# Performance work log

Hardware: AMD Instinct MI355X
Metric: run time of the kernel (lower is better)

## Reference

```python
import jax, jax.numpy as jnp
import numpy as np

B, S, H, E, TOP_K = 4, 4096, 4096, 64, 2

def setup_inputs() -> dict:
    key = jax.random.key(0)
    k1, k2 = jax.random.split(key)
    hidden_states = jax.random.normal(k1, (B, S, H), dtype=jnp.float32)
    gate_weight = jax.random.normal(k2, (E, H), dtype=jnp.float32) * (H ** -0.5)
    return {"hidden_states": hidden_states, "gate_weight": gate_weight}

def reference(hidden_states, gate_weight):
    # gate: logits[b,s,e] = hidden[b,s,h] @ W[e,h]^T (nn.Linear, no bias)
    router_logits = jnp.einsum('bsh,eh->bse', hidden_states, gate_weight)
    router_probs = jax.nn.softmax(router_logits, axis=-1)
    # top-k over experts, then renormalize the selected weights
    expert_weights, expert_indices = jax.lax.top_k(router_probs, TOP_K)
    expert_weights = expert_weights / jnp.sum(expert_weights, axis=-1, keepdims=True)
    return (router_probs, expert_indices, expert_weights)
```

## Files before the change

kernel.cpp:

```cpp
#include <hip/hip_runtime.h>
#include <math.h>

#define TOKENS 16384
#define HDIM 4096
#define NE 64

#define BM 64
#define BK 64
#define LP 68

typedef float f32x4 __attribute__((ext_vector_type(4)));
typedef int i32x4 __attribute__((ext_vector_type(4)));
typedef __bf16 bf16x8 __attribute__((ext_vector_type(8)));

__device__ __forceinline__ void split8(f32x4 v0, f32x4 v1, i32x4& h, i32x4& l) {
  float x[8];
#pragma unroll
  for (int j = 0; j < 4; ++j) { x[j] = v0[j]; x[4 + j] = v1[j]; }
  union { unsigned short u[8]; i32x4 v; } H, L;
#pragma unroll
  for (int j = 0; j < 8; ++j) {
    __bf16 hb = (__bf16)x[j];
    H.u[j] = __builtin_bit_cast(unsigned short, hb);
    L.u[j] = __builtin_bit_cast(unsigned short, (__bf16)(x[j] - (float)hb));
  }
  h = H.v; l = L.v;
}

__device__ __forceinline__ f32x4 mfma_bf16(i32x4 a, i32x4 b, f32x4 c) {
  return __builtin_amdgcn_mfma_f32_16x16x32_bf16(
      __builtin_bit_cast(bf16x8, a), __builtin_bit_cast(bf16x8, b), c, 0, 0, 0);
}

__global__ __launch_bounds__(256) void convert_w(const float* __restrict__ W,
                                                 unsigned short* __restrict__ Wh,
                                                 unsigned short* __restrict__ Wl) {
  const int i = (blockIdx.x * 256 + threadIdx.x) * 8;
  f32x4 v0 = *(const f32x4*)(W + i);
  f32x4 v1 = *(const f32x4*)(W + i + 4);
  i32x4 h, l;
  split8(v0, v1, h, l);
  *(i32x4*)(Wh + i) = h;
  *(i32x4*)(Wl + i) = l;
}

__global__ __launch_bounds__(512, 2) void router_mfma(const float* __restrict__ A,
                                                      const unsigned short* __restrict__ Wh,
                                                      const unsigned short* __restrict__ Wl,
                                                      float* __restrict__ out) {
  __shared__ __align__(16) unsigned short smem[4 * BM * BK];
  unsigned short* AhS = smem;
  unsigned short* AlS = smem + BM * BK;
  unsigned short* WhS = smem + 2 * BM * BK;
  unsigned short* WlS = smem + 3 * BM * BK;

  const int tid = threadIdx.x;
  const int bt = blockIdx.x;

  const int srow = tid >> 3;
  const int sc = tid & 7;
  const int soff = srow * BK + ((sc ^ (srow & 7)) << 3);

  const float* Ab = A + (size_t)(bt * BM + srow) * HDIM + sc * 8;
  const unsigned short* Whb = Wh + srow * HDIM + sc * 8;
  const unsigned short* Wlb = Wl + srow * HDIM + sc * 8;

  const int lane = tid & 63;
  const int wv = tid >> 6;
  const int tg = wv & 3;
  const int eg = wv >> 2;
  const int l15 = lane & 15;
  const int l7 = lane & 7;
  const int fko = lane >> 4;
  const int arow = tg * 16 + l15;
  const int brow = eg * 32 + l15;

  f32x4 acc0 = {0.f, 0.f, 0.f, 0.f};
  f32x4 acc1 = {0.f, 0.f, 0.f, 0.f};

  f32x4 a0 = *(const f32x4*)(Ab);
  f32x4 a1 = *(const f32x4*)(Ab + 4);
  i32x4 whr = *(const i32x4*)(Whb);
  i32x4 wlr = *(const i32x4*)(Wlb);

  for (int kc = BK;; kc += BK) {
    i32x4 ah, al;
    split8(a0, a1, ah, al);
    *(i32x4*)&AhS[soff] = ah;
    *(i32x4*)&AlS[soff] = al;
    *(i32x4*)&WhS[soff] = whr;
    *(i32x4*)&WlS[soff] = wlr;
    __syncthreads();

    if (kc < HDIM) {
      a0 = *(const f32x4*)(Ab + kc);
      a1 = *(const f32x4*)(Ab + kc + 4);
      whr = *(const i32x4*)(Whb + kc);
      wlr = *(const i32x4*)(Wlb + kc);
    }

#pragma unroll
    for (int ks = 0; ks < 2; ++ks) {
      const int ch = ks * 4 + fko;
      const int aoff = arow * BK + ((ch ^ l7) << 3);
      const int boff = brow * BK + ((ch ^ l7) << 3);
      i32x4 fah = *(const i32x4*)&AhS[aoff];
      i32x4 fal = *(const i32x4*)&AlS[aoff];
      i32x4 fbh0 = *(const i32x4*)&WhS[boff];
      i32x4 fbl0 = *(const i32x4*)&WlS[boff];
      i32x4 fbh1 = *(const i32x4*)&WhS[boff + 16 * BK];
      i32x4 fbl1 = *(const i32x4*)&WlS[boff + 16 * BK];
      acc0 = mfma_bf16(fah, fbh0, acc0);
      acc1 = mfma_bf16(fah, fbh1, acc1);
      acc0 = mfma_bf16(fal, fbh0, acc0);
      acc1 = mfma_bf16(fal, fbh1, acc1);
      acc0 = mfma_bf16(fah, fbl0, acc0);
      acc1 = mfma_bf16(fah, fbl1, acc1);
      acc0 = mfma_bf16(fal, fbl0, acc0);
      acc1 = mfma_bf16(fal, fbl1, acc1);
    }
    if (kc >= HDIM) break;
    __syncthreads();
  }

  __syncthreads();
  float* L = (float*)smem;
#pragma unroll
  for (int r = 0; r < 4; ++r) {
    const int row = tg * 16 + fko * 4 + r;
    L[row * LP + eg * 32 + l15] = acc0[r];
    L[row * LP + eg * 32 + 16 + l15] = acc1[r];
  }
  __syncthreads();

  const int wv8 = tid >> 6;
#pragma unroll
  for (int r = 0; r < 8; ++r) {
    const int lt = wv8 * 8 + r;
    const int tok = bt * BM + lt;
    const float l = L[lt * LP + lane];

    float m = l;
#pragma unroll
    for (int off = 32; off >= 1; off >>= 1) m = fmaxf(m, __shfl_xor(m, off, 64));

    const float e = expf(l - m);
    float sum = e;
#pragma unroll
    for (int off = 32; off >= 1; off >>= 1) sum += __shfl_xor(sum, off, 64);

    const float p = e / sum;
    out[(size_t)tok * NE + lane] = p;

    float m0 = p;
#pragma unroll
    for (int off = 32; off >= 1; off >>= 1) m0 = fmaxf(m0, __shfl_xor(m0, off, 64));
    const unsigned long long b0 = __ballot(p == m0);
    const int i0 = __ffsll(b0) - 1;

    const float pm = (lane == i0) ? -1.f : p;
    float m1 = pm;
#pragma unroll
    for (int off = 32; off >= 1; off >>= 1) m1 = fmaxf(m1, __shfl_xor(m1, off, 64));
    const unsigned long long b1 = __ballot(pm == m1);
    const int i1 = __ffsll(b1) - 1;

    if (lane == 0) {
      float* idxo = out + (size_t)TOKENS * NE + (size_t)tok * 2;
      idxo[0] = (float)i0;
      idxo[1] = (float)i1;
      float* wo = out + (size_t)TOKENS * NE + (size_t)TOKENS * 2 + (size_t)tok * 2;
      const float d = m0 + m1;
      wo[0] = m0 / d;
      wo[1] = m1 / d;
    }
  }
}

extern "C" void kernel_launch(void* const* d_in, const int* in_sizes, int n_in,
                              void* d_out, int out_size, void* d_ws, size_t ws_size,
                              hipStream_t stream) {
  const float* A = (const float*)d_in[0];
  const float* W = (const float*)d_in[1];
  float* out = (float*)d_out;
  unsigned short* Whi = (unsigned short*)d_ws;
  unsigned short* Wlo = Whi + (size_t)NE * HDIM;

  convert_w<<<dim3(NE * HDIM / (256 * 8)), 256, 0, stream>>>(W, Whi, Wlo);
  router_mfma<<<dim3(TOKENS / BM), 512, 0, stream>>>(A, Whi, Wlo, out);
}
```

Before: 395.6 us.

## Double-buffer LDS tiles and drop lo*lo MFMA term in split-bf16 GEMM

Changes the router GEMM main loop to ping-pong between two LDS buffers. Staging the next tile overlaps with MFMA on the current one, which cuts the barrier count per K-step from two to one. It also removes the low×low bf16 product from the three-term split, so each step issues 6 MFMAs instead of 8. That slightly lowers accuracy, and the doubled LDS (64KB per block) may reduce occupancy.

```diff
diff --git a/kernel.cpp b/kernel.cpp
--- a/kernel.cpp
+++ b/kernel.cpp
@@ -7,7 +7,9 @@
 
 #define BM 64
 #define BK 64
+#define NT (HDIM / BK)
 #define LP 68
+#define TSZ (BM * BK)
 
 typedef float f32x4 __attribute__((ext_vector_type(4)));
 typedef int i32x4 __attribute__((ext_vector_type(4)));
@@ -48,11 +50,9 @@
                                                       const unsigned short* __restrict__ Wh,
                                                       const unsigned short* __restrict__ Wl,
                                                       float* __restrict__ out) {
-  __shared__ __align__(16) unsigned short smem[4 * BM * BK];
-  unsigned short* AhS = smem;
-  unsigned short* AlS = smem + BM * BK;
-  unsigned short* WhS = smem + 2 * BM * BK;
-  unsigned short* WlS = smem + 3 * BM * BK;
+  __shared__ __align__(16) unsigned short smem[2 * 4 * TSZ];
+  unsigned short* buf0 = smem;
+  unsigned short* buf1 = smem + 4 * TSZ;
 
   const int tid = threadIdx.x;
   const int bt = blockIdx.x;
@@ -78,27 +78,31 @@
   f32x4 acc0 = {0.f, 0.f, 0.f, 0.f};
   f32x4 acc1 = {0.f, 0.f, 0.f, 0.f};
 
-  f32x4 a0 = *(const f32x4*)(Ab);
-  f32x4 a1 = *(const f32x4*)(Ab + 4);
-  i32x4 whr = *(const i32x4*)(Whb);
-  i32x4 wlr = *(const i32x4*)(Wlb);
-
-  for (int kc = BK;; kc += BK) {
-    i32x4 ah, al;
-    split8(a0, a1, ah, al);
-    *(i32x4*)&AhS[soff] = ah;
-    *(i32x4*)&AlS[soff] = al;
-    *(i32x4*)&WhS[soff] = whr;
-    *(i32x4*)&WlS[soff] = wlr;
-    __syncthreads();
-
-    if (kc < HDIM) {
-      a0 = *(const f32x4*)(Ab + kc);
-      a1 = *(const f32x4*)(Ab + kc + 4);
-      whr = *(const i32x4*)(Whb + kc);
-      wlr = *(const i32x4*)(Wlb + kc);
-    }
-
+  f32x4 a0_0, a1_0, a0_1, a1_1;
+  i32x4 wh_0, wl_0, wh_1, wl_1;
+
+  auto loadS = [&](int t, f32x4& a0, f32x4& a1, i32x4& wh, i32x4& wl) {
+    const int kc = t * BK;
+    a0 = *(const f32x4*)(Ab + kc);
+    a1 = *(const f32x4*)(Ab + kc + 4);
+    wh = *(const i32x4*)(Whb + kc);
+    wl = *(const i32x4*)(Wlb + kc);
+  };
+
+  auto stage = [&](unsigned short* B, f32x4 a0, f32x4 a1, i32x4 wh, i32x4 wl) {
+    i32x4 h, l;
+    split8(a0, a1, h, l);
+    *(i32x4*)&B[soff] = h;
+    *(i32x4*)&B[TSZ + soff] = l;
+    *(i32x4*)&B[2 * TSZ + soff] = wh;
+    *(i32x4*)&B[3 * TSZ + soff] = wl;
+  };
+
+  auto compute = [&](const unsigned short* B) {
+    const unsigned short* AhS = B;
+    const unsigned short* AlS = B + TSZ;
+    const unsigned short* WhS = B + 2 * TSZ;
+    const unsigned short* WlS = B + 3 * TSZ;
 #pragma unroll
     for (int ks = 0; ks < 2; ++ks) {
       const int ch = ks * 4 + fko;
@@ -107,8 +111,8 @@
       i32x4 fah = *(const i32x4*)&AhS[aoff];
       i32x4 fal = *(const i32x4*)&AlS[aoff];
       i32x4 fbh0 = *(const i32x4*)&WhS[boff];
+      i32x4 fbh1 = *(const i32x4*)&WhS[boff + 16 * BK];
       i32x4 fbl0 = *(const i32x4*)&WlS[boff];
-      i32x4 fbh1 = *(const i32x4*)&WhS[boff + 16 * BK];
       i32x4 fbl1 = *(const i32x4*)&WlS[boff + 16 * BK];
       acc0 = mfma_bf16(fah, fbh0, acc0);
       acc1 = mfma_bf16(fah, fbh1, acc1);
@@ -116,14 +120,26 @@
       acc1 = mfma_bf16(fal, fbh1, acc1);
       acc0 = mfma_bf16(fah, fbl0, acc0);
       acc1 = mfma_bf16(fah, fbl1, acc1);
-      acc0 = mfma_bf16(fal, fbl0, acc0);
-      acc1 = mfma_bf16(fal, fbl1, acc1);
     }
-    if (kc >= HDIM) break;
+  };
+
+  loadS(0, a0_0, a1_0, wh_0, wl_0);
+  stage(buf0, a0_0, a1_0, wh_0, wl_0);
+  loadS(1, a0_1, a1_1, wh_1, wl_1);
+  __syncthreads();
+
+  for (int t = 0; t < NT; t += 2) {
+    compute(buf0);
+    if (t + 2 < NT) loadS(t + 2, a0_0, a1_0, wh_0, wl_0);
+    stage(buf1, a0_1, a1_1, wh_1, wl_1);
     __syncthreads();
-  }
-
-  __syncthreads();
+
+    compute(buf1);
+    if (t + 3 < NT) loadS(t + 3, a0_1, a1_1, wh_1, wl_1);
+    if (t + 2 < NT) stage(buf0, a0_0, a1_0, wh_0, wl_0);
+    __syncthreads();
+  }
+
   float* L = (float*)smem;
 #pragma unroll
   for (int r = 0; r < 4; ++r) {
```

New measurement: 394.2 us. About the same (-0.4%).

## Load MFMA fragments directly from global memory, drop LDS staging and low-low term

Applied to the files above, without the earlier changes.

Replaces the LDS-staged, double-synchronised K loop with per-wave direct global loads of A and W fragments into MFMA operand registers, removing shared-memory writes, reads and barriers. It also drops the lo*lo bf16 product, cutting MFMAs per step from 8 to 6. In exchange A is fetched and split by two waves, W is reread by four waves, global access is less coalesced, and the split-bf16 accuracy drops slightly.

```diff
diff --git a/kernel.cpp b/kernel.cpp
--- a/kernel.cpp
+++ b/kernel.cpp
@@ -6,7 +6,6 @@
 #define NE 64
 
 #define BM 64
-#define BK 64
 #define LP 68
 
 typedef float f32x4 __attribute__((ext_vector_type(4)));
@@ -48,83 +47,44 @@
                                                       const unsigned short* __restrict__ Wh,
                                                       const unsigned short* __restrict__ Wl,
                                                       float* __restrict__ out) {
-  __shared__ __align__(16) unsigned short smem[4 * BM * BK];
-  unsigned short* AhS = smem;
-  unsigned short* AlS = smem + BM * BK;
-  unsigned short* WhS = smem + 2 * BM * BK;
-  unsigned short* WlS = smem + 3 * BM * BK;
+  __shared__ __align__(16) float L[BM * LP];
 
   const int tid = threadIdx.x;
   const int bt = blockIdx.x;
-
-  const int srow = tid >> 3;
-  const int sc = tid & 7;
-  const int soff = srow * BK + ((sc ^ (srow & 7)) << 3);
-
-  const float* Ab = A + (size_t)(bt * BM + srow) * HDIM + sc * 8;
-  const unsigned short* Whb = Wh + srow * HDIM + sc * 8;
-  const unsigned short* Wlb = Wl + srow * HDIM + sc * 8;
-
   const int lane = tid & 63;
   const int wv = tid >> 6;
   const int tg = wv & 3;
   const int eg = wv >> 2;
   const int l15 = lane & 15;
-  const int l7 = lane & 7;
   const int fko = lane >> 4;
-  const int arow = tg * 16 + l15;
-  const int brow = eg * 32 + l15;
+
+  const float* Ap = A + (size_t)(bt * BM + tg * 16 + l15) * HDIM + fko * 8;
+  const unsigned short* Wh0 = Wh + (size_t)(eg * 32 + l15) * HDIM + fko * 8;
+  const unsigned short* Wl0 = Wl + (size_t)(eg * 32 + l15) * HDIM + fko * 8;
+  const unsigned short* Wh1 = Wh0 + 16 * HDIM;
+  const unsigned short* Wl1 = Wl0 + 16 * HDIM;
 
   f32x4 acc0 = {0.f, 0.f, 0.f, 0.f};
   f32x4 acc1 = {0.f, 0.f, 0.f, 0.f};
 
-  f32x4 a0 = *(const f32x4*)(Ab);
-  f32x4 a1 = *(const f32x4*)(Ab + 4);
-  i32x4 whr = *(const i32x4*)(Whb);
-  i32x4 wlr = *(const i32x4*)(Wlb);
-
-  for (int kc = BK;; kc += BK) {
+#pragma unroll 2
+  for (int kc = 0; kc < HDIM; kc += 32) {
+    f32x4 a0 = *(const f32x4*)(Ap + kc);
+    f32x4 a1 = *(const f32x4*)(Ap + kc + 4);
+    i32x4 wh0 = *(const i32x4*)(Wh0 + kc);
+    i32x4 wh1 = *(const i32x4*)(Wh1 + kc);
+    i32x4 wl0 = *(const i32x4*)(Wl0 + kc);
+    i32x4 wl1 = *(const i32x4*)(Wl1 + kc);
     i32x4 ah, al;
     split8(a0, a1, ah, al);
-    *(i32x4*)&AhS[soff] = ah;
-    *(i32x4*)&AlS[soff] = al;
-    *(i32x4*)&WhS[soff] = whr;
-    *(i32x4*)&WlS[soff] = wlr;
-    __syncthreads();
-
-    if (kc < HDIM) {
-      a0 = *(const f32x4*)(Ab + kc);
-      a1 = *(const f32x4*)(Ab + kc + 4);
-      whr = *(const i32x4*)(Whb + kc);
-      wlr = *(const i32x4*)(Wlb + kc);
-    }
-
-#pragma unroll
-    for (int ks = 0; ks < 2; ++ks) {
-      const int ch = ks * 4 + fko;
-      const int aoff = arow * BK + ((ch ^ l7) << 3);
-      const int boff = brow * BK + ((ch ^ l7) << 3);
-      i32x4 fah = *(const i32x4*)&AhS[aoff];
-      i32x4 fal = *(const i32x4*)&AlS[aoff];
-      i32x4 fbh0 = *(const i32x4*)&WhS[boff];
-      i32x4 fbl0 = *(const i32x4*)&WlS[boff];
-      i32x4 fbh1 = *(const i32x4*)&WhS[boff + 16 * BK];
-      i32x4 fbl1 = *(const i32x4*)&WlS[boff + 16 * BK];
-      acc0 = mfma_bf16(fah, fbh0, acc0);
-      acc1 = mfma_bf16(fah, fbh1, acc1);
-      acc0 = mfma_bf16(fal, fbh0, acc0);
-      acc1 = mfma_bf16(fal, fbh1, acc1);
-      acc0 = mfma_bf16(fah, fbl0, acc0);
-      acc1 = mfma_bf16(fah, fbl1, acc1);
-      acc0 = mfma_bf16(fal, fbl0, acc0);
-      acc1 = mfma_bf16(fal, fbl1, acc1);
-    }
-    if (kc >= HDIM) break;
-    __syncthreads();
+    acc0 = mfma_bf16(ah, wh0, acc0);
+    acc1 = mfma_bf16(ah, wh1, acc1);
+    acc0 = mfma_bf16(al, wh0, acc0);
+    acc1 = mfma_bf16(al, wh1, acc1);
+    acc0 = mfma_bf16(ah, wl0, acc0);
+    acc1 = mfma_bf16(ah, wl1, acc1);
   }
 
-  __syncthreads();
-  float* L = (float*)smem;
 #pragma unroll
   for (int r = 0; r < 4; ++r) {
     const int row = tg * 16 + fko * 4 + r;
```

Measured after the change: 476.4 us. 1.2x slower.
